# Performance work log

Measured on AMD Instinct MI355X. Metric: run time of the kernel, lower is better.

Reference implementation:

```python
import jax, jax.numpy as jnp
import numpy as np

D_MODEL = 1024
NHEAD = 16
HEAD_DIM = D_MODEL // NHEAD  # 64
THETA = 10000.0


def apply_rope(t):
    # t: [B, H, S, D]. Interleaved-pair RoPE (lucidrains rotary-embedding-torch
    # rotate_queries_or_keys), positions = arange(S), theta = 10000.
    B, H, S, D = t.shape
    inv_freq = 1.0 / (THETA ** (jnp.arange(0, D, 2, dtype=jnp.float32) / D))  # [D/2]
    ang = jnp.arange(S, dtype=jnp.float32)[:, None] * inv_freq               # [S, D/2]
    cos = jnp.cos(ang).astype(t.dtype)
    sin = jnp.sin(ang).astype(t.dtype)
    tp = t.reshape(B, H, S, D // 2, 2)
    x1, x2 = tp[..., 0], tp[..., 1]
    rot = jnp.stack([x1 * cos - x2 * sin, x1 * sin + x2 * cos], axis=-1)
    return rot.reshape(B, H, S, D)


def setup_inputs() -> dict:
    key = jax.random.key(0)
    k0, k1, k2, k3, k4 = jax.random.split(key, 5)
    B, Sx, Sc = 2, 2048, 2048
    sc = 0.02  # weight init scale
    return {
        "x": jax.random.normal(k0, (B, Sx, D_MODEL), jnp.float32),
        "context": jax.random.normal(k1, (B, Sc, D_MODEL), jnp.float32),
        "Wq": jax.random.normal(k2, (D_MODEL, D_MODEL), jnp.float32) * sc,
        "Wv": jax.random.normal(k3, (D_MODEL, D_MODEL), jnp.float32) * sc,
        "Wo": jax.random.normal(k4, (D_MODEL, D_MODEL), jnp.float32) * sc,
        "bo": jnp.zeros((D_MODEL,), jnp.float32),
        "x_pos": jnp.arange(B * Sx, dtype=jnp.int64).reshape(B, Sx) % Sx,
        "context_pos": jnp.arange(B * Sc, dtype=jnp.int64).reshape(B, Sc) % Sc,
    }


def reference(x, context, Wq, Wv, Wo, bo, x_pos, context_pos):
    # x_pos/context_pos are unused when both streams use the internal
    # RotaryEmbedding (is_imu1=is_imu2=True), matching the original forward.
    B, Sx, _ = x.shape
    Sc = context.shape[1]
    q = (x @ Wq.T).reshape(B, Sx, NHEAD, HEAD_DIM).transpose(0, 2, 1, 3)
    # NOTE: original code uses projq (not projk) for keys — replicated here.
    k = (context @ Wq.T).reshape(B, Sc, NHEAD, HEAD_DIM).transpose(0, 2, 1, 3)
    v = (context @ Wv.T).reshape(B, Sc, NHEAD, HEAD_DIM).transpose(0, 2, 1, 3)
    q = apply_rope(q)
    k = apply_rope(k)
    scale = 1.0 / jnp.sqrt(jnp.asarray(HEAD_DIM, q.dtype))
    attn = jax.nn.softmax(jnp.einsum("bhqd,bhkd->bhqk", q, k) * scale, axis=-1)
    out = jnp.einsum("bhqk,bhkd->bhqd", attn, v)            # [B,H,Sx,hd]
    out = out.transpose(0, 2, 1, 3).reshape(B, Sx, D_MODEL)  # [B,Sx,d_model]
    return out @ Wo.T + bo
```

## Files before the change

### kernel.cpp

```cpp
#include <hip/hip_runtime.h>
#include <cmath>


typedef __bf16 bf16x8 __attribute__((ext_vector_type(8)));
typedef __bf16 bf16x4 __attribute__((ext_vector_type(4)));
typedef float f32x4 __attribute__((ext_vector_type(4)));

#define MFMA(A, B, C) __builtin_amdgcn_mfma_f32_16x16x32_bf16(A, B, C, 0, 0, 0)
#define GLL16(g, l)                                                        \
  __builtin_amdgcn_global_load_lds(                                        \
      (const __attribute__((address_space(1))) unsigned int*)(g),          \
      (__attribute__((address_space(3))) unsigned int*)(l), 16, 0, 0)

__global__ __launch_bounds__(256) void cvt_all_kernel(
    const float* __restrict__ x, const float* __restrict__ ctx,
    const float* __restrict__ Wq, const float* __restrict__ Wv,
    const float* __restrict__ Wo, __bf16* __restrict__ xb, __bf16* __restrict__ cb,
    __bf16* __restrict__ Wqb, __bf16* __restrict__ Wvb, __bf16* __restrict__ Wob) {
  int i = blockIdx.x * 256 + threadIdx.x;
  const float* src;
  __bf16* dst;
  int off;
  if (i < 1048576) { src = x; dst = xb; off = 0; }
  else if (i < 2097152) { src = ctx; dst = cb; off = 1048576; }
  else if (i < 2359296) { src = Wq; dst = Wqb; off = 2097152; }
  else if (i < 2621440) { src = Wv; dst = Wvb; off = 2359296; }
  else { src = Wo; dst = Wob; off = 2621440; }
  int j = i - off;
  float4 f = ((const float4*)src)[j];
  bf16x4 o;
  o[0] = (__bf16)f.x; o[1] = (__bf16)f.y; o[2] = (__bf16)f.z; o[3] = (__bf16)f.w;
  ((bf16x4*)dst)[j] = o;
}

template <int MODE>
__global__ __launch_bounds__(256) void gemm_bt(const __bf16* __restrict__ A0,
                                               const __bf16* __restrict__ W0,
                                               void* __restrict__ outp0,
                                               void* __restrict__ outp1,
                                               void* __restrict__ outp2,
                                               const float* __restrict__ bias) {
  const int tid = threadIdx.x;
  const int wave = tid >> 6, lane = tid & 63, quad = lane >> 4, l15 = lane & 15;
  const int mw = wave >> 1, nw = wave & 1;
  const int n0 = blockIdx.y * 128;

  int m0 = blockIdx.x * 128;
  const __bf16* A = A0;
  const __bf16* W = W0;
  bool vmode = false;
  if (MODE == 0 && blockIdx.x >= 64) {
    m0 = (blockIdx.x - 64) * 128;
    A = A0 + (size_t)4096 * 1024;
    W = W0 + (size_t)1024 * 1024;
    vmode = true;
  }

  __shared__ __attribute__((aligned(16))) __bf16 As[2][4096];
  __shared__ __attribute__((aligned(16))) __bf16 Ws[2][4096];

  int goff[2];
#pragma unroll
  for (int jj = 0; jj < 2; jj++) {
    const int s = jj * 256 + tid;
    const int row = s >> 2;
    const int kcg = (s & 3) ^ ((row >> 1) & 3);
    goff[jj] = row * 1024 + kcg * 8;
  }
  const __bf16* Ag = A + (size_t)m0 * 1024;
  const __bf16* Wg = W + (size_t)n0 * 1024;
  const int ldsoff0 = (0 * 256 + wave * 64) * 8;
  const int ldsoff1 = (1 * 256 + wave * 64) * 8;

  const int sw = (l15 >> 1) & 3;
  int afoff[4], wfoff[4];
#pragma unroll
  for (int t = 0; t < 4; t++) {
    afoff[t] = (mw * 64 + t * 16 + l15) * 32 + (quad ^ sw) * 8;
    wfoff[t] = (nw * 64 + t * 16 + l15) * 32 + (quad ^ sw) * 8;
  }

  f32x4 acc[4][4] = {};

  auto stage = [&](int buf, int k0) {
    GLL16(Ag + goff[0] + k0, &As[buf][ldsoff0]);
    GLL16(Ag + goff[1] + k0, &As[buf][ldsoff1]);
    GLL16(Wg + goff[0] + k0, &Ws[buf][ldsoff0]);
    GLL16(Wg + goff[1] + k0, &Ws[buf][ldsoff1]);
  };
  auto compute = [&](int buf) {
    bf16x8 af[4], wf[4];
#pragma unroll
    for (int t = 0; t < 4; t++) af[t] = *(const bf16x8*)&As[buf][afoff[t]];
#pragma unroll
    for (int t = 0; t < 4; t++) wf[t] = *(const bf16x8*)&Ws[buf][wfoff[t]];
#pragma unroll
    for (int mt = 0; mt < 4; mt++)
#pragma unroll
      for (int nt = 0; nt < 4; nt++) acc[mt][nt] = MFMA(af[mt], wf[nt], acc[mt][nt]);
  };

  stage(0, 0);
  for (int k0 = 0; k0 < 1024; k0 += 64) {
    __syncthreads();
    if (k0 + 32 < 1024) stage(1, k0 + 32);
    compute(0);
    __syncthreads();
    if (k0 + 64 < 1024) stage(0, k0 + 64);
    compute(1);
  }

  if (MODE == 0) {
    if (!vmode) {
      const int stream = (m0 >= 4096);
      __bf16* O = (__bf16*)(stream ? outp1 : outp0);
      const float qsc = stream ? 1.0f : 0.18033688f;
      const int mb = m0 & 4095;
#pragma unroll
      for (int nt = 0; nt < 4; nt++) {
        const int n = n0 + nw * 64 + nt * 16 + l15;
        const int h = n >> 6, d = n & 63, p = d >> 1;
        const float invf = __builtin_amdgcn_exp2f(-(float)p * 0.41524101f);
#pragma unroll
        for (int mt = 0; mt < 4; mt++) {
#pragma unroll
          for (int r = 0; r < 4; r++) {
            const int row = mb + mw * 64 + mt * 16 + quad * 4 + r;
            const int s = row & 2047, b = row >> 11;
            float v = acc[mt][nt][r];
            float pv = __shfl_xor(v, 1, 64);
            float sn, cs;
            __sincosf((float)s * invf, &sn, &cs);
            float res = (lane & 1) ? (pv * sn + v * cs) : (v * cs - pv * sn);
            O[((size_t)(b * 16 + h) * 2048 + s) * 64 + d] = (__bf16)(res * qsc);
          }
        }
      }
    } else {
      __bf16* O = (__bf16*)outp2;
#pragma unroll
      for (int nt = 0; nt < 4; nt++) {
        const int n = n0 + nw * 64 + nt * 16 + l15;
        const int h = n >> 6, d = n & 63;
#pragma unroll
        for (int mt = 0; mt < 4; mt++) {
          const int rowb = m0 + mw * 64 + mt * 16 + quad * 4;
          const int s = rowb & 2047, b = rowb >> 11;
          bf16x4 o;
#pragma unroll
          for (int r = 0; r < 4; r++) o[r] = (__bf16)acc[mt][nt][r];
          *(bf16x4*)(O + ((size_t)(b * 16 + h) * 64 + d) * 2048 + s) = o;
        }
      }
    }
  } else {
    float* O = (float*)outp0;
#pragma unroll
    for (int nt = 0; nt < 4; nt++) {
      const int n = n0 + nw * 64 + nt * 16 + l15;
      const float bv = bias[n];
#pragma unroll
      for (int mt = 0; mt < 4; mt++) {
#pragma unroll
        for (int r = 0; r < 4; r++) {
          const int row = m0 + mw * 64 + mt * 16 + quad * 4 + r;
          O[(size_t)row * 1024 + n] = acc[mt][nt][r] + bv;
        }
      }
    }
  }
}

__global__ __launch_bounds__(256) void attn_kernel(const __bf16* __restrict__ Q,
                                                   const __bf16* __restrict__ K,
                                                   const __bf16* __restrict__ Vt,
                                                   __bf16* __restrict__ Aout) {
  const int tid = threadIdx.x;
  const int wave = tid >> 6, lane = tid & 63, quad = lane >> 4, l15 = lane & 15;
  const int q0 = blockIdx.x * 64;
  const int bh = blockIdx.y;

  const __bf16* Qb = Q + (size_t)bh * (2048 * 64);
  const __bf16* Kb = K + (size_t)bh * (2048 * 64);
  const __bf16* Vb = Vt + (size_t)bh * (64 * 2048);

  __shared__ __attribute__((aligned(16))) __bf16 Kbuf[2][4096];
  __shared__ __attribute__((aligned(16))) __bf16 Vbuf[2][4096];
  __shared__ __attribute__((aligned(16))) __bf16 Plds[4][8][16][8];

  const __bf16* qp = Qb + (size_t)(q0 + wave * 16 + l15) * 64 + quad * 8;
  const bf16x8 qf0 = *(const bf16x8*)qp;
  const bf16x8 qf1 = *(const bf16x8*)(qp + 32);

  const int s0 = (wave * 2 + 0) * 64 + lane;
  const int s1 = (wave * 2 + 1) * 64 + lane;
  const int r0 = s0 >> 3, c0 = (s0 & 7) ^ (r0 & 7);
  const int r1 = s1 >> 3, c1 = (s1 & 7) ^ (r1 & 7);
  const __bf16* kg0 = Kb + r0 * 64 + c0 * 8;
  const __bf16* kg1 = Kb + r1 * 64 + c1 * 8;
  const __bf16* vg0 = Vb + r0 * 2048 + c0 * 8;
  const __bf16* vg1 = Vb + r1 * 2048 + c1 * 8;
  const int kldsA = (wave * 2 + 0) * 512;
  const int kldsB = (wave * 2 + 1) * 512;

  const int offF0 = l15 * 64 + ((quad ^ (l15 & 7)) * 8);
  const int offF1 = l15 * 64 + (((4 + quad) ^ (l15 & 7)) * 8);

  float rsum = 0.f;
  f32x4 oT[4] = {};

  auto stage = [&](int buf, int kt) {
    GLL16(kg0 + kt * 64, &Kbuf[buf][kldsA]);
    GLL16(kg1 + kt * 64, &Kbuf[buf][kldsB]);
    GLL16(vg0 + kt, &Vbuf[buf][kldsA]);
    GLL16(vg1 + kt, &Vbuf[buf][kldsB]);
  };
  auto compute = [&](int buf) {
    f32x4 sT[4];
#pragma unroll
    for (int nt = 0; nt < 4; nt++) {
      bf16x8 kf0 = *(const bf16x8*)&Kbuf[buf][nt * 1024 + offF0];
      bf16x8 kf1 = *(const bf16x8*)&Kbuf[buf][nt * 1024 + offF1];
      f32x4 z = {};
      z = MFMA(kf0, qf0, z);
      sT[nt] = MFMA(kf1, qf1, z);
    }
#pragma unroll
    for (int nt = 0; nt < 4; nt++) {
      bf16x4 pb;
#pragma unroll
      for (int r = 0; r < 4; r++) {
        float pe = __builtin_amdgcn_exp2f(sT[nt][r]);
        rsum += pe;
        pb[r] = (__bf16)pe;
      }
      const int chunk = nt * 2 + (quad >> 1);
      *(bf16x4*)&Plds[wave][chunk][l15 ^ ((chunk & 3) << 1)][(quad & 1) * 4] = pb;
    }
    bf16x8 pf0 = *(const bf16x8*)&Plds[wave][quad][l15 ^ (quad << 1)][0];
    bf16x8 pf1 = *(const bf16x8*)&Plds[wave][4 + quad][l15 ^ (quad << 1)][0];
#pragma unroll
    for (int nt = 0; nt < 4; nt++) {
      bf16x8 vf0 = *(const bf16x8*)&Vbuf[buf][nt * 1024 + offF0];
      bf16x8 vf1 = *(const bf16x8*)&Vbuf[buf][nt * 1024 + offF1];
      oT[nt] = MFMA(vf0, pf0, oT[nt]);
      oT[nt] = MFMA(vf1, pf1, oT[nt]);
    }
  };

  stage(0, 0);
  for (int kt = 0; kt < 2048; kt += 128) {
    __syncthreads();
    if (kt + 64 < 2048) stage(1, kt + 64);
    compute(0);
    __syncthreads();
    if (kt + 128 < 2048) stage(0, kt + 128);
    compute(1);
  }

  const int b = bh >> 4, h = bh & 15;
  float l = rsum;
  l += __shfl_xor(l, 16, 64);
  l += __shfl_xor(l, 32, 64);
  const float inv = 1.f / l;
  const int q = q0 + wave * 16 + l15;
#pragma unroll
  for (int nt = 0; nt < 4; nt++) {
    bf16x4 o;
#pragma unroll
    for (int r = 0; r < 4; r++) o[r] = (__bf16)(oT[nt][r] * inv);
    *(bf16x4*)&Aout[((size_t)(b * 2048 + q)) * 1024 + h * 64 + nt * 16 + quad * 4] = o;
  }
}

extern "C" void kernel_launch(void* const* d_in, const int* in_sizes, int n_in,
                              void* d_out, int out_size, void* d_ws, size_t ws_size,
                              hipStream_t stream) {
  const float* x   = (const float*)d_in[0];
  const float* ctx = (const float*)d_in[1];
  const float* Wq  = (const float*)d_in[2];
  const float* Wv  = (const float*)d_in[3];
  const float* Wo  = (const float*)d_in[4];
  const float* bo  = (const float*)d_in[5];

  char* ws = (char*)d_ws;
  const size_t MB = 1024 * 1024;
  __bf16* xb   = (__bf16*)(ws + 0 * MB);
  __bf16* cb   = (__bf16*)(ws + 8 * MB);
  __bf16* Wqb  = (__bf16*)(ws + 16 * MB);
  __bf16* Wvb  = (__bf16*)(ws + 18 * MB);
  __bf16* Wob  = (__bf16*)(ws + 20 * MB);
  __bf16* qh   = (__bf16*)(ws + 22 * MB);
  __bf16* kh   = (__bf16*)(ws + 30 * MB);
  __bf16* vt   = (__bf16*)(ws + 38 * MB);
  __bf16* attn = xb;

  cvt_all_kernel<<<11264, 256, 0, stream>>>(x, ctx, Wq, Wv, Wo, xb, cb, Wqb, Wvb, Wob);

  gemm_bt<0><<<dim3(96, 8), 256, 0, stream>>>(xb, Wqb, (void*)qh, (void*)kh,
                                              (void*)vt, nullptr);

  attn_kernel<<<dim3(32, 32), 256, 0, stream>>>(qh, kh, vt, attn);

  gemm_bt<2><<<dim3(32, 8), 256, 0, stream>>>(attn, Wob, d_out, nullptr, nullptr, bo);
}
```

Measured before the change: 221.6 us.

## Split GEMM into projection and smaller-tile output kernels, remap attention grid, cheaper RoPE trig

Replaces the templated GEMM with a dedicated projection kernel and a separate output-projection kernel that uses 64x64 tiles. This raises the output GEMM's block count from 256 to 1024 so the GPU's CUs are better filled. The attention launch becomes a 1D grid whose blocks are remapped so consecutive blocks go to different (batch, head) pairs, likely to spread load across XCDs and caches. RoPE now uses hardware sin/cos on a fractional revolution count instead of __sincosf, which may cost a little accuracy at large angles.

```diff
diff --git a/kernel.cpp b/kernel.cpp
--- a/kernel.cpp
+++ b/kernel.cpp
@@ -33,13 +33,11 @@
   ((bf16x4*)dst)[j] = o;
 }
 
-template <int MODE>
-__global__ __launch_bounds__(256) void gemm_bt(const __bf16* __restrict__ A0,
-                                               const __bf16* __restrict__ W0,
-                                               void* __restrict__ outp0,
-                                               void* __restrict__ outp1,
-                                               void* __restrict__ outp2,
-                                               const float* __restrict__ bias) {
+__global__ __launch_bounds__(256) void gemm_proj(const __bf16* __restrict__ A0,
+                                                 const __bf16* __restrict__ W0,
+                                                 void* __restrict__ outQ,
+                                                 void* __restrict__ outK,
+                                                 void* __restrict__ outV) {
   const int tid = threadIdx.x;
   const int wave = tid >> 6, lane = tid & 63, quad = lane >> 4, l15 = lane & 15;
   const int mw = wave >> 1, nw = wave & 1;
@@ -49,7 +47,7 @@
   const __bf16* A = A0;
   const __bf16* W = W0;
   bool vmode = false;
-  if (MODE == 0 && blockIdx.x >= 64) {
+  if (blockIdx.x >= 64) {
     m0 = (blockIdx.x - 64) * 128;
     A = A0 + (size_t)4096 * 1024;
     W = W0 + (size_t)1024 * 1024;
@@ -69,8 +67,8 @@
   }
   const __bf16* Ag = A + (size_t)m0 * 1024;
   const __bf16* Wg = W + (size_t)n0 * 1024;
-  const int ldsoff0 = (0 * 256 + wave * 64) * 8;
-  const int ldsoff1 = (1 * 256 + wave * 64) * 8;
+  const int ldsoff0 = wave * 512;
+  const int ldsoff1 = 2048 + wave * 512;
 
   const int sw = (l15 >> 1) & 3;
   int afoff[4], wfoff[4];
@@ -110,62 +108,116 @@
     compute(1);
   }
 
-  if (MODE == 0) {
-    if (!vmode) {
-      const int stream = (m0 >= 4096);
-      __bf16* O = (__bf16*)(stream ? outp1 : outp0);
-      const float qsc = stream ? 1.0f : 0.18033688f;
-      const int mb = m0 & 4095;
-#pragma unroll
-      for (int nt = 0; nt < 4; nt++) {
-        const int n = n0 + nw * 64 + nt * 16 + l15;
-        const int h = n >> 6, d = n & 63, p = d >> 1;
-        const float invf = __builtin_amdgcn_exp2f(-(float)p * 0.41524101f);
-#pragma unroll
-        for (int mt = 0; mt < 4; mt++) {
-#pragma unroll
-          for (int r = 0; r < 4; r++) {
-            const int row = mb + mw * 64 + mt * 16 + quad * 4 + r;
-            const int s = row & 2047, b = row >> 11;
-            float v = acc[mt][nt][r];
-            float pv = __shfl_xor(v, 1, 64);
-            float sn, cs;
-            __sincosf((float)s * invf, &sn, &cs);
-            float res = (lane & 1) ? (pv * sn + v * cs) : (v * cs - pv * sn);
-            O[((size_t)(b * 16 + h) * 2048 + s) * 64 + d] = (__bf16)(res * qsc);
-          }
+  if (!vmode) {
+    const int isK = (m0 >= 4096);
+    __bf16* O = (__bf16*)(isK ? outK : outQ);
+    const float qsc = isK ? 1.0f : 0.18033688f;
+    const int mb = m0 & 4095;
+#pragma unroll
+    for (int nt = 0; nt < 4; nt++) {
+      const int n = n0 + nw * 64 + nt * 16 + l15;
+      const int h = n >> 6, d = n & 63, p = d >> 1;
+      const float invf_rev =
+          __builtin_amdgcn_exp2f(-((float)p * 0.41524101f + 2.6514961f));
+#pragma unroll
+      for (int mt = 0; mt < 4; mt++) {
+#pragma unroll
+        for (int r = 0; r < 4; r++) {
+          const int row = mb + mw * 64 + mt * 16 + quad * 4 + r;
+          const int s = row & 2047, b = row >> 11;
+          float v = acc[mt][nt][r];
+          float pv = __shfl_xor(v, 1, 64);
+          float fr = __builtin_amdgcn_fractf((float)s * invf_rev);
+          float sn = __builtin_amdgcn_sinf(fr);
+          float cs = __builtin_amdgcn_cosf(fr);
+          float res = (lane & 1) ? (pv * sn + v * cs) : (v * cs - pv * sn);
+          O[((size_t)(b * 16 + h) * 2048 + s) * 64 + d] = (__bf16)(res * qsc);
         }
       }
-    } else {
-      __bf16* O = (__bf16*)outp2;
-#pragma unroll
-      for (int nt = 0; nt < 4; nt++) {
-        const int n = n0 + nw * 64 + nt * 16 + l15;
-        const int h = n >> 6, d = n & 63;
-#pragma unroll
-        for (int mt = 0; mt < 4; mt++) {
-          const int rowb = m0 + mw * 64 + mt * 16 + quad * 4;
-          const int s = rowb & 2047, b = rowb >> 11;
-          bf16x4 o;
-#pragma unroll
-          for (int r = 0; r < 4; r++) o[r] = (__bf16)acc[mt][nt][r];
-          *(bf16x4*)(O + ((size_t)(b * 16 + h) * 64 + d) * 2048 + s) = o;
-        }
+    }
+  } else {
+    __bf16* O = (__bf16*)outV;
+#pragma unroll
+    for (int nt = 0; nt < 4; nt++) {
+      const int n = n0 + nw * 64 + nt * 16 + l15;
+      const int h = n >> 6, d = n & 63;
+#pragma unroll
+      for (int mt = 0; mt < 4; mt++) {
+        const int rowb = m0 + mw * 64 + mt * 16 + quad * 4;
+        const int s = rowb & 2047, b = rowb >> 11;
+        bf16x4 o;
+#pragma unroll
+        for (int r = 0; r < 4; r++) o[r] = (__bf16)acc[mt][nt][r];
+        *(bf16x4*)(O + ((size_t)(b * 16 + h) * 64 + d) * 2048 + s) = o;
       }
     }
-  } else {
-    float* O = (float*)outp0;
-#pragma unroll
-    for (int nt = 0; nt < 4; nt++) {
-      const int n = n0 + nw * 64 + nt * 16 + l15;
-      const float bv = bias[n];
-#pragma unroll
-      for (int mt = 0; mt < 4; mt++) {
-#pragma unroll
-        for (int r = 0; r < 4; r++) {
-          const int row = m0 + mw * 64 + mt * 16 + quad * 4 + r;
-          O[(size_t)row * 1024 + n] = acc[mt][nt][r] + bv;
-        }
+  }
+}
+
+__global__ __launch_bounds__(256) void gemm_out(const __bf16* __restrict__ A,
+                                                const __bf16* __restrict__ W,
+                                                float* __restrict__ O,
+                                                const float* __restrict__ bias) {
+  const int tid = threadIdx.x;
+  const int wave = tid >> 6, lane = tid & 63, quad = lane >> 4, l15 = lane & 15;
+  const int mw = wave >> 1, nw = wave & 1;
+  const int m0 = blockIdx.x * 64, n0 = blockIdx.y * 64;
+
+  __shared__ __attribute__((aligned(16))) __bf16 As[2][2048];
+  __shared__ __attribute__((aligned(16))) __bf16 Ws[2][2048];
+
+  const int srow = tid >> 2;
+  const int goff = srow * 1024 + (((tid & 3) ^ ((srow >> 1) & 3)) * 8);
+  const __bf16* Ag = A + (size_t)m0 * 1024;
+  const __bf16* Wg = W + (size_t)n0 * 1024;
+  const int ldsoff = wave * 512;
+
+  const int sw = (l15 >> 1) & 3;
+  int afoff[2], wfoff[2];
+#pragma unroll
+  for (int t = 0; t < 2; t++) {
+    afoff[t] = (mw * 32 + t * 16 + l15) * 32 + (quad ^ sw) * 8;
+    wfoff[t] = (nw * 32 + t * 16 + l15) * 32 + (quad ^ sw) * 8;
+  }
+
+  f32x4 acc[2][2] = {};
+
+  auto stage = [&](int buf, int k0) {
+    GLL16(Ag + goff + k0, &As[buf][ldsoff]);
+    GLL16(Wg + goff + k0, &Ws[buf][ldsoff]);
+  };
+  auto compute = [&](int buf) {
+    bf16x8 af[2], wf[2];
+#pragma unroll
+    for (int t = 0; t < 2; t++) af[t] = *(const bf16x8*)&As[buf][afoff[t]];
+#pragma unroll
+    for (int t = 0; t < 2; t++) wf[t] = *(const bf16x8*)&Ws[buf][wfoff[t]];
+#pragma unroll
+    for (int mt = 0; mt < 2; mt++)
+#pragma unroll
+      for (int nt = 0; nt < 2; nt++) acc[mt][nt] = MFMA(af[mt], wf[nt], acc[mt][nt]);
+  };
+
+  stage(0, 0);
+  for (int k0 = 0; k0 < 1024; k0 += 64) {
+    __syncthreads();
+    if (k0 + 32 < 1024) stage(1, k0 + 32);
+    compute(0);
+    __syncthreads();
+    if (k0 + 64 < 1024) stage(0, k0 + 64);
+    compute(1);
+  }
+
+#pragma unroll
+  for (int nt = 0; nt < 2; nt++) {
+    const int n = n0 + nw * 32 + nt * 16 + l15;
+    const float bv = bias[n];
+#pragma unroll
+    for (int mt = 0; mt < 2; mt++) {
+#pragma unroll
+      for (int r = 0; r < 4; r++) {
+        const int row = m0 + mw * 32 + mt * 16 + quad * 4 + r;
+        O[(size_t)row * 1024 + n] = acc[mt][nt][r] + bv;
       }
     }
   }
@@ -177,8 +229,10 @@
                                                    __bf16* __restrict__ Aout) {
   const int tid = threadIdx.x;
   const int wave = tid >> 6, lane = tid & 63, quad = lane >> 4, l15 = lane & 15;
-  const int q0 = blockIdx.x * 64;
-  const int bh = blockIdx.y;
+  const int id = blockIdx.x;
+  const int j = id >> 3;
+  const int bh = ((id & 7) << 2) | (j & 3);
+  const int q0 = (j >> 2) << 6;
 
   const __bf16* Qb = Q + (size_t)bh * (2048 * 64);
   const __bf16* Kb = K + (size_t)bh * (2048 * 64);
@@ -297,10 +351,9 @@
 
   cvt_all_kernel<<<11264, 256, 0, stream>>>(x, ctx, Wq, Wv, Wo, xb, cb, Wqb, Wvb, Wob);
 
-  gemm_bt<0><<<dim3(96, 8), 256, 0, stream>>>(xb, Wqb, (void*)qh, (void*)kh,
-                                              (void*)vt, nullptr);
-
-  attn_kernel<<<dim3(32, 32), 256, 0, stream>>>(qh, kh, vt, attn);
-
-  gemm_bt<2><<<dim3(32, 8), 256, 0, stream>>>(attn, Wob, d_out, nullptr, nullptr, bo);
-}
+  gemm_proj<<<dim3(96, 8), 256, 0, stream>>>(xb, Wqb, (void*)qh, (void*)kh, (void*)vt);
+
+  attn_kernel<<<1024, 256, 0, stream>>>(qh, kh, vt, attn);
+
+  gemm_out<<<dim3(64, 16), 256, 0, stream>>>(attn, Wob, (float*)d_out, bo);
+}
```

New measurement: 218.0 us. About the same (-1.6%).
